# Optimization experiments

Measured on AMD Instinct MI355X. Metric: run time of the kernel, lower is better.

## Reference

```python
import jax, jax.numpy as jnp
import numpy as np

H = 16        # query heads
D = 4         # KV downsampling -> H//D = 4 kv heads
WINDOW = 1024 # sliding window
THETA = 10000.0


def _rope_cos_sin(L, dim):
    freqs = 1.0 / (THETA ** (jnp.arange(0, dim - 1, 2, dtype=jnp.float32) / dim))
    ang = jnp.arange(L, dtype=jnp.float32)[:, None] * freqs[None, :]  # (L, dim//2)
    return jnp.cos(ang), jnp.sin(ang)


def _apply_rope(x, cos, sin):
    # x: (N, h, L, dim); interleaved complex pairs (even=real, odd=imag)
    xr, xi = x[..., 0::2], x[..., 1::2]
    orr = xr * cos - xi * sin
    oii = xr * sin + xi * cos
    return jnp.stack([orr, oii], axis=-1).reshape(x.shape)


def setup_inputs() -> dict:
    key = jax.random.key(0)
    ks = jax.random.split(key, 5)
    N, L, E = 4, 2048, 2048
    return {
        "x": jax.random.normal(ks[0], (N, L, E), dtype=jnp.float32),
        "Wq": jax.random.normal(ks[1], (E, E), dtype=jnp.float32) * 0.02,
        "Wk": jax.random.normal(ks[2], (E // D, E), dtype=jnp.float32) * 0.02,
        "Wv": jax.random.normal(ks[3], (E // D, E), dtype=jnp.float32) * 0.02,
        "Wo": jax.random.normal(ks[4], (E, E), dtype=jnp.float32) * 0.02,
    }


def reference(x, Wq, Wk, Wv, Wo):
    N, L, E = x.shape
    dim = E // H  # 128 per-head dim (same for q and downsampled k/v)
    Hkv = H // D

    q = (x @ Wq.T).reshape(N, L, H, dim).transpose(0, 2, 1, 3)      # (N,H,L,d)
    k = (x @ Wk.T).reshape(N, L, Hkv, dim).transpose(0, 2, 1, 3)    # (N,Hkv,L,d)
    v = (x @ Wv.T).reshape(N, L, Hkv, dim).transpose(0, 2, 1, 3)

    cos, sin = _rope_cos_sin(L, dim)
    q = _apply_rope(q, cos, sin)
    k = _apply_rope(k, cos, sin)

    # GQA: expand kv heads (repeat_interleave along head axis)
    k = jnp.repeat(k, D, axis=1)  # (N,H,L,d)
    v = jnp.repeat(v, D, axis=1)

    scale = 1.0 / jnp.sqrt(jnp.float32(dim))
    attn = jnp.einsum("bhld,bhsd->bhls", q, k) * scale  # (N,H,L,L)

    i = jnp.arange(L)[:, None]
    j = jnp.arange(L)[None, :]
    allowed = (j <= i) & (j > i - WINDOW)  # causal + sliding window
    attn = jnp.where(allowed[None, None], attn, -jnp.inf)
    attn = jax.nn.softmax(attn, axis=-1)

    z = jnp.einsum("bhls,bhsd->bhld", attn, v)  # (N,H,L,d)
    z = z.transpose(0, 2, 1, 3).reshape(N, L, E)
    return z @ Wo.T
```

## Files before the change

### kernel.cpp

```cpp
#include <hip/hip_runtime.h>
#include <hip/hip_bf16.h>
#include <math.h>

typedef unsigned short u16;
typedef unsigned int u32;
typedef __attribute__((ext_vector_type(8))) short short8;
typedef __attribute__((ext_vector_type(8))) u16 ushort8;
typedef __attribute__((ext_vector_type(4))) float f32x4;
typedef __attribute__((ext_vector_type(16))) float f32x16;
typedef __attribute__((ext_vector_type(4))) u32 u32x4;

#define N_B 4
#define L_S 2048
#define E_D 2048
#define NH 16
#define HD 128
#define WIN 1024
#define QW 3072
#define LOG2E 1.4426950408889634f

static __device__ __forceinline__ u16 f32_bf16(float f) {
  u32 u = __builtin_bit_cast(u32, f);
  u = (u + 0x7fffu + ((u >> 16) & 1u)) >> 16;
  return (u16)u;
}
static __device__ __forceinline__ float bf16_f32(u16 h) {
  u32 u = ((u32)h) << 16;
  return __builtin_bit_cast(float, u);
}
static __device__ __forceinline__ u32 pack_bf16_pair(float lo, float hi) {
  __hip_bfloat162 h2 = __float22bfloat162_rn(make_float2(lo, hi));
  u32 r;
  __builtin_memcpy(&r, &h2, 4);
  return r;
}
static __device__ __forceinline__ void gload_lds16(const void* g, void* l) {
  __builtin_amdgcn_global_load_lds((__attribute__((address_space(1))) void*)g,
                                   (__attribute__((address_space(3))) void*)l, 16, 0, 0);
}

__global__ void k_cast(const float* __restrict__ src, u16* __restrict__ dst, int n8) {
  int i = blockIdx.x * blockDim.x + threadIdx.x;
  if (i >= n8) return;
  const float4* s = (const float4*)src + (size_t)i * 2;
  float4 a = s[0], b = s[1];
  ushort8 v;
  v[0] = f32_bf16(a.x); v[1] = f32_bf16(a.y); v[2] = f32_bf16(a.z); v[3] = f32_bf16(a.w);
  v[4] = f32_bf16(b.x); v[5] = f32_bf16(b.y); v[6] = f32_bf16(b.z); v[7] = f32_bf16(b.w);
  *((ushort8*)dst + i) = v;
}

__global__ void k_cast_w(const float* __restrict__ Wq, const float* __restrict__ Wk,
                         const float* __restrict__ Wv, const float* __restrict__ Wo,
                         u16* __restrict__ Wqkv, u16* __restrict__ Wob,
                         float* __restrict__ cs, float* __restrict__ sn) {
  int bb = blockIdx.x;
  if (bb >= 5120) {
    int idx = (bb - 5120) * 256 + threadIdx.x;
    int l = idx >> 6, f = idx & 63;
    float freq = exp2f(-(float)f * (13.287712379549449f / 64.0f));
    float ang = (float)l * freq;
    cs[idx] = cosf(ang);
    sn[idx] = sinf(ang);
    return;
  }
  const float* src;
  u16* dst;
  int base;
  if (bb < 2048)      { src = Wq; dst = Wqkv;                 base = bb; }
  else if (bb < 2560) { src = Wk; dst = Wqkv + 2048 * 2048;   base = bb - 2048; }
  else if (bb < 3072) { src = Wv; dst = Wqkv + 2560 * 2048;   base = bb - 2560; }
  else                { src = Wo; dst = Wob;                  base = bb - 3072; }
  int i = base * 256 + threadIdx.x;
  const float4* s = (const float4*)src + (size_t)i * 2;
  float4 a = s[0], b = s[1];
  ushort8 v;
  v[0] = f32_bf16(a.x); v[1] = f32_bf16(a.y); v[2] = f32_bf16(a.z); v[3] = f32_bf16(a.w);
  v[4] = f32_bf16(b.x); v[5] = f32_bf16(b.y); v[6] = f32_bf16(b.z); v[7] = f32_bf16(b.w);
  *((ushort8*)dst + i) = v;
}

__global__ void k_rope_k(u16* __restrict__ QKV, const float* __restrict__ cs,
                         const float* __restrict__ sn) {
  int idx = blockIdx.x * blockDim.x + threadIdx.x;
  int f = idx & 63;
  int rest = idx >> 6;
  int hh = rest & 3;
  int row = rest >> 2;
  int l = row & (L_S - 1);
  int col = E_D + hh * HD + 2 * f;
  u32* p = (u32*)(QKV + (size_t)row * QW + col);
  u32 v = *p;
  float xr = bf16_f32((u16)(v & 0xffffu));
  float xi = bf16_f32((u16)(v >> 16));
  float c = cs[l * 64 + f], s = sn[l * 64 + f];
  float orr = xr * c - xi * s;
  float oii = xr * s + xi * c;
  *p = (u32)f32_bf16(orr) | ((u32)f32_bf16(oii) << 16);
}

template <int OUT_F32, int BN>
__global__ __launch_bounds__(512, 1) void k_gemm8(
    const u16* __restrict__ A, int lda,
    const u16* __restrict__ B, int ldb,
    void* __restrict__ Cp, int ldc, int K) {
  constexpr int NF = BN / 64;
  constexpr int PB = BN / 128;
  constexpr int BBY = BN * 64;
  constexpr int LVM = 2 + PB;
  __shared__ __align__(16) u16 Ab[3 * 8192];
  __shared__ __align__(16) u16 Bb[3 * (BN * 32)];
  const int tid = threadIdx.x;
  const int lane = tid & 63, w = tid >> 6;
  const int lr = lane & 15, lg = lane >> 4;
  const int wm = w >> 2, wn = w & 3;
  const int fid = blockIdx.x;
  const int cc = fid & 7, l = fid >> 3;
  const int m0 = (cc * 4 + (l & 3)) * 256;
  const int n0 = (l >> 2) * BN;
  const int rswz = (lr & 6) << 3;

  const int r2 = tid >> 2;
  const int ce = (((tid & 3) * 16) ^ ((r2 & 6) << 3)) >> 1;
  auto STAGE_A = [&](int kt, int bb) {
#pragma unroll
    for (int rr = 0; rr < 2; ++rr)
      gload_lds16(A + (size_t)(m0 + rr * 128 + r2) * lda + kt * 32 + ce,
                  (char*)Ab + bb * 16384 + rr * 8192 + (w << 10));
  };
  auto STAGE_B = [&](int kt, int bb) {
#pragma unroll
    for (int rr = 0; rr < PB; ++rr)
      gload_lds16(B + (size_t)(n0 + rr * 128 + r2) * ldb + kt * 32 + ce,
                  (char*)Bb + bb * BBY + rr * 8192 + (w << 10));
  };

  f32x4 acc[8][NF];
  const f32x4 z4 = {0.f, 0.f, 0.f, 0.f};
#pragma unroll
  for (int mf = 0; mf < 8; ++mf)
#pragma unroll
    for (int nf = 0; nf < NF; ++nf) acc[mf][nf] = z4;

  const int nt = K >> 5;
  STAGE_A(0, 0); STAGE_B(0, 0);
  STAGE_A(1, 1); STAGE_B(1, 1);
  asm volatile("s_waitcnt vmcnt(%0)" :: "i"(LVM) : "memory");
  __builtin_amdgcn_sched_barrier(0);
  __builtin_amdgcn_s_barrier();
  __builtin_amdgcn_sched_barrier(0);

  int c3 = 0;
  for (int t = 0; t < nt; ++t) {
    int ib = c3 + 2; if (ib >= 3) ib -= 3;
    const char* Abt = (const char*)Ab + c3 * 16384;
    const char* Bbt = (const char*)Bb + c3 * BBY;
    short8 af[4], bf[NF];
#pragma unroll
    for (int nf = 0; nf < NF; ++nf) {
      int row = wn * (BN / 4) + nf * 16 + lr;
      bf[nf] = *(const short8*)(Bbt + row * 64 + ((lg * 16) ^ rswz));
    }
#pragma unroll
    for (int mf = 0; mf < 4; ++mf) {
      int row = wm * 128 + mf * 16 + lr;
      af[mf] = *(const short8*)(Abt + row * 64 + ((lg * 16) ^ rswz));
    }
    if (t + 2 < nt) STAGE_A(t + 2, ib);
    __builtin_amdgcn_sched_barrier(0);
    __builtin_amdgcn_s_barrier();
    asm volatile("s_waitcnt lgkmcnt(0)" ::: "memory");
    __builtin_amdgcn_sched_barrier(0);
    __builtin_amdgcn_s_setprio(1);
#pragma unroll
    for (int mf = 0; mf < 4; ++mf)
#pragma unroll
      for (int nf = 0; nf < NF; ++nf)
        acc[mf][nf] =
            __builtin_amdgcn_mfma_f32_16x16x32_bf16(af[mf], bf[nf], acc[mf][nf], 0, 0, 0);
    __builtin_amdgcn_s_setprio(0);
    __builtin_amdgcn_sched_barrier(0);
    __builtin_amdgcn_s_barrier();
    __builtin_amdgcn_sched_barrier(0);
#pragma unroll
    for (int mf = 0; mf < 4; ++mf) {
      int row = wm * 128 + 64 + mf * 16 + lr;
      af[mf] = *(const short8*)(Abt + row * 64 + ((lg * 16) ^ rswz));
    }
    if (t + 2 < nt) STAGE_B(t + 2, ib);
    if (t + 2 < nt)
      asm volatile("s_waitcnt vmcnt(%0)" :: "i"(LVM) : "memory");
    else
      asm volatile("s_waitcnt vmcnt(0)" ::: "memory");
    __builtin_amdgcn_sched_barrier(0);
    __builtin_amdgcn_s_barrier();
    asm volatile("s_waitcnt lgkmcnt(0)" ::: "memory");
    __builtin_amdgcn_sched_barrier(0);
    __builtin_amdgcn_s_setprio(1);
#pragma unroll
    for (int mf = 0; mf < 4; ++mf)
#pragma unroll
      for (int nf = 0; nf < NF; ++nf)
        acc[4 + mf][nf] =
            __builtin_amdgcn_mfma_f32_16x16x32_bf16(af[mf], bf[nf], acc[4 + mf][nf], 0, 0, 0);
    __builtin_amdgcn_s_setprio(0);
    __builtin_amdgcn_sched_barrier(0);
    __builtin_amdgcn_s_barrier();
    __builtin_amdgcn_sched_barrier(0);
    c3 = (c3 == 2) ? 0 : c3 + 1;
  }

#pragma unroll
  for (int mf = 0; mf < 8; ++mf)
#pragma unroll
    for (int nf = 0; nf < NF; ++nf)
#pragma unroll
      for (int j = 0; j < 4; ++j) {
        size_t r = (size_t)(m0 + wm * 128 + mf * 16 + lg * 4 + j);
        int c = n0 + wn * (BN / 4) + nf * 16 + lr;
        if (OUT_F32)
          ((float*)Cp)[r * ldc + c] = acc[mf][nf][j];
        else
          ((u16*)Cp)[r * ldc + c] = f32_bf16(acc[mf][nf][j]);
      }
}

__global__ __launch_bounds__(512, 2) void k_attn(u16* __restrict__ QKV,
                                                 const float* __restrict__ cs,
                                                 const float* __restrict__ sn) {
  const int bx = blockIdx.x, h = blockIdx.y, b = blockIdx.z;
  const int qb = (b >= 2) ? 7 - bx : bx;
  const int tid = threadIdx.x;
  const int lane = tid & 63, w = tid >> 6;
  const int l31 = lane & 31, hi = lane >> 5;
  const int kh = h >> 2;
  const int qs = qb * 256 + w * 32;
  __shared__ __align__(16) u16 Klds[2][64 * 128];
  __shared__ __align__(16) u16 Vt[2][128 * 64];
  const float SCL2 = 0.08838834764831845f * 1.4426950408889634f;
  const size_t bL = (size_t)b * L_S;
  const int q = qs + l31;
  const size_t rowQ = (bL + q) * QW + h * HD;
  short8 qf[8];
#pragma unroll
  for (int ds = 0; ds < 8; ++ds) {
    short8 qr = *(const short8*)(QKV + rowQ + ds * 16 + hi * 8);
    const int f0 = ds * 8 + hi * 4;
    float4 c4 = *(const float4*)(cs + (size_t)q * 64 + f0);
    float4 s4 = *(const float4*)(sn + (size_t)q * 64 + f0);
    ushort8 qo;
#pragma unroll
    for (int e = 0; e < 4; ++e) {
      float xr = bf16_f32((u16)qr[2 * e]);
      float xi = bf16_f32((u16)qr[2 * e + 1]);
      float co = (e == 0) ? c4.x : (e == 1) ? c4.y : (e == 2) ? c4.z : c4.w;
      float si = (e == 0) ? s4.x : (e == 1) ? s4.y : (e == 2) ? s4.z : s4.w;
      qo[2 * e]     = f32_bf16(xr * co - xi * si);
      qo[2 * e + 1] = f32_bf16(xr * si + xi * co);
    }
    qf[ds] = __builtin_bit_cast(short8, qo);
  }
  f32x16 o[4];
#pragma unroll
  for (int dt = 0; dt < 4; ++dt)
#pragma unroll
    for (int r = 0; r < 16; ++r) o[dt][r] = 0.f;
  float m2 = -3e38f, lsum = 0.f;
  int t0 = qb * 256 - (WIN - 1);
  if (t0 < 0) t0 = 0;
  t0 >>= 6;
  const int t1 = 4 * qb + 3;
  short8 vreg[2];

  auto ISSUE_K = [&](int t, int buf) {
    char* Kb = (char*)Klds + buf * 16384;
#pragma unroll
    for (int rr = 0; rr < 2; ++rr) {
      int row = rr * 32 + (tid >> 4);
      int colb = ((tid & 15) * 16) ^ ((row & 7) << 4);
      gload_lds16(QKV + (bL + t * 64 + row) * QW + E_D + kh * HD + (colb >> 1),
                  Kb + rr * 8192 + w * 1024 + (lane << 4));
    }
  };
  auto LOAD_V = [&](int t) {
#pragma unroll
    for (int rr = 0; rr < 2; ++rr)
      vreg[rr] = *(const short8*)(QKV + (bL + t * 64 + lane) * QW + E_D + 512 + kh * HD +
                                  ((w * 2 + rr) * 8));
  };
  auto WRITE_V = [&](int buf) {
    char* Vb = (char*)Vt + buf * 16384;
#pragma unroll
    for (int rr = 0; rr < 2; ++rr) {
      int db = (w * 2 + rr) * 8;
#pragma unroll
      for (int e = 0; e < 8; ++e)
        *(u16*)(Vb + ((((db + e) * 128) + lane * 2) ^ (e << 4))) = (u16)vreg[rr][e];
    }
  };

  LOAD_V(t0);
  ISSUE_K(t0, 0);
  __syncthreads();
  WRITE_V(0);
  int c = 0;

  for (int t = t0; t <= t1; ++t) {
    const int kv0 = t * 64;
    const bool lastt = (t == t1);
    if (!lastt) {
      ISSUE_K(t + 1, c ^ 1);
      LOAD_V(t + 1);
    }
    const bool act = (kv0 <= qs + 31) && (kv0 + 63 > qs - WIN);
    const bool full = (kv0 + 63 <= qs) && (kv0 > qs + 31 - WIN);
    u32x4 pa[4];
    if (act) {
      char* Kb = (char*)Klds + c * 16384;
      f32x16 s[2];
#pragma unroll
      for (int g = 0; g < 2; ++g)
#pragma unroll
        for (int r = 0; r < 16; ++r) s[g][r] = 0.f;
#pragma unroll
      for (int g = 0; g < 2; ++g) {
        const int r = g * 32 + l31;
        const int rsw = (r & 7) << 4;
#pragma unroll
        for (int ds = 0; ds < 8; ++ds) {
          short8 kf = *(const short8*)(Kb + (r * 256 + ((ds * 32 + hi * 16) ^ rsw)));
          s[g] = __builtin_amdgcn_mfma_f32_32x32x16_bf16(kf, qf[ds], s[g], 0, 0, 0);
        }
      }
      float v[2][16];
      float mx = -3e38f;
      if (full) {
#pragma unroll
        for (int g = 0; g < 2; ++g)
#pragma unroll
          for (int r = 0; r < 16; ++r) {
            float vv = s[g][r] * SCL2;
            v[g][r] = vv;
            mx = fmaxf(mx, vv);
          }
      } else {
#pragma unroll
        for (int g = 0; g < 2; ++g)
#pragma unroll
          for (int r = 0; r < 16; ++r) {
            int kg = kv0 + g * 32 + (r & 3) + 8 * (r >> 2) + 4 * hi;
            bool a = (kg <= q) && (kg > q - WIN);
            float vv = a ? s[g][r] * SCL2 : -3e38f;
            v[g][r] = vv;
            mx = fmaxf(mx, vv);
          }
      }
      mx = fmaxf(mx, __shfl_xor(mx, 32));
      if (__ballot(mx > m2 + 11.5415603f)) {
        float mn = fmaxf(m2, mx);
        float alpha = exp2f(m2 - mn);
        m2 = mn;
        lsum *= alpha;
#pragma unroll
        for (int r = 0; r < 16; ++r) {
          float alr = __shfl(alpha, (r & 3) + 8 * (r >> 2) + 4 * hi);
#pragma unroll
          for (int dt = 0; dt < 4; ++dt) o[dt][r] *= alr;
        }
      }
      float rs = 0.f;
      if (full) {
#pragma unroll
        for (int g = 0; g < 2; ++g)
#pragma unroll
          for (int r = 0; r < 16; ++r) {
            float pe = exp2f(v[g][r] - m2);
            v[g][r] = pe;
            rs += pe;
          }
      } else {
#pragma unroll
        for (int g = 0; g < 2; ++g)
#pragma unroll
          for (int r = 0; r < 16; ++r) {
            float pe = (v[g][r] > -1e37f) ? exp2f(v[g][r] - m2) : 0.f;
            v[g][r] = pe;
            rs += pe;
          }
      }
      rs += __shfl_xor(rs, 32);
      lsum += rs;
#pragma unroll
      for (int g = 0; g < 2; ++g) {
        u32 W[8];
#pragma unroll
        for (int qi = 0; qi < 4; ++qi) {
          W[2 * qi]     = pack_bf16_pair(v[g][4 * qi + 0], v[g][4 * qi + 1]);
          W[2 * qi + 1] = pack_bf16_pair(v[g][4 * qi + 2], v[g][4 * qi + 3]);
        }
        u32 R[4];
        R[0] = __shfl_xor(hi ? W[0] : W[2], 32);
        R[1] = __shfl_xor(hi ? W[1] : W[3], 32);
        R[2] = __shfl_xor(hi ? W[4] : W[6], 32);
        R[3] = __shfl_xor(hi ? W[5] : W[7], 32);
#pragma unroll
        for (int ksl = 0; ksl < 2; ++ksl) {
          u32x4 fr;
          if (hi == 0) {
            fr[0] = W[4 * ksl]; fr[1] = W[4 * ksl + 1];
            fr[2] = R[2 * ksl]; fr[3] = R[2 * ksl + 1];
          } else {
            fr[0] = R[2 * ksl]; fr[1] = R[2 * ksl + 1];
            fr[2] = W[4 * ksl + 2]; fr[3] = W[4 * ksl + 3];
          }
          pa[g * 2 + ksl] = fr;
        }
      }
    }
    __syncthreads();
    if (act) {
      char* Vb = (char*)Vt + c * 16384;
      __builtin_amdgcn_s_setprio(1);
#pragma unroll
      for (int dt = 0; dt < 4; ++dt) {
        const int d = dt * 32 + l31;
        const int dsw = (d & 7) << 4;
#pragma unroll
        for (int ks = 0; ks < 4; ++ks) {
          short8 vf = *(const short8*)(Vb + (d * 128 + ((ks * 32 + hi * 16) ^ dsw)));
          o[dt] = __builtin_amdgcn_mfma_f32_32x32x16_bf16(
              __builtin_bit_cast(short8, pa[ks]), vf, o[dt], 0, 0, 0);
        }
      }
      __builtin_amdgcn_s_setprio(0);
    }
    if (!lastt) WRITE_V(c ^ 1);
    c ^= 1;
  }
  float inv = 1.0f / lsum;
#pragma unroll
  for (int r = 0; r < 16; ++r) {
    int ridx = (r & 3) + 8 * (r >> 2) + 4 * hi;
    float invr = __shfl(inv, ridx);
    size_t rowO = (bL + qs + ridx) * QW + h * HD + l31;
#pragma unroll
    for (int dt = 0; dt < 4; ++dt)
      QKV[rowO + dt * 32] = f32_bf16(o[dt][r] * invr);
  }
}

extern "C" void kernel_launch(void* const* d_in, const int* in_sizes, int n_in,
                              void* d_out, int out_size, void* d_ws, size_t ws_size,
                              hipStream_t stream) {
  const float* x  = (const float*)d_in[0];
  const float* Wq = (const float*)d_in[1];
  const float* Wk = (const float*)d_in[2];
  const float* Wv = (const float*)d_in[3];
  const float* Wo = (const float*)d_in[4];
  char* ws = (char*)d_ws;
  if (ws_size < 105906176u) return;
  u16* xb    = (u16*)(ws);
  u16* Wqkv  = (u16*)(ws + 33554432);
  u16* Wob   = (u16*)(ws + 46137344);
  u16* QKV   = (u16*)(ws + 54525952);
  float* cs  = (float*)(ws + 104857600);
  float* sn  = (float*)(ws + 105381888);

  k_cast<<<8192, 256, 0, stream>>>(x, xb, 16777216 / 8);
  k_cast_w<<<5632, 256, 0, stream>>>(Wq, Wk, Wv, Wo, Wqkv, Wob, cs, sn);
  k_gemm8<0, 128><<<768, 512, 0, stream>>>(xb, 2048, Wqkv, 2048, QKV, QW, 2048);
  k_rope_k<<<8192, 256, 0, stream>>>(QKV, cs, sn);
  k_attn<<<dim3(8, 16, 4), 512, 0, stream>>>(QKV, cs, sn);
  k_gemm8<1, 256><<<256, 512, 0, stream>>>(QKV, QW, Wob, 2048, d_out, 2048, 2048);
}
```

Before: 351.4 us.

## Triple-buffer K tiles and single-buffer V with explicit vmcnt waits

Moves the attention kernel's K tile staging from double to triple buffering, so K is prefetched two tiles ahead via direct-to-LDS loads. V shrinks to a single LDS buffer, written after a second barrier. The full __syncthreads is replaced by manual s_waitcnt with partial vmcnt counts and raw s_barrier calls, so in-flight K loads need not drain at each iteration. This aims to hide global latency better, but it adds a barrier per iteration and depends on exact vmcnt accounting being correct.

```diff
diff --git a/kernel.cpp b/kernel.cpp
--- a/kernel.cpp
+++ b/kernel.cpp
@@ -235,8 +235,9 @@
   const int l31 = lane & 31, hi = lane >> 5;
   const int kh = h >> 2;
   const int qs = qb * 256 + w * 32;
-  __shared__ __align__(16) u16 Klds[2][64 * 128];
-  __shared__ __align__(16) u16 Vt[2][128 * 64];
+  __shared__ __align__(16) u16 Klds[3][64 * 128];
+  __shared__ __align__(16) u16 Vt[128 * 64];
+  char* Vb = (char*)Vt;
   const float SCL2 = 0.08838834764831845f * 1.4426950408889634f;
   const size_t bL = (size_t)b * L_S;
   const int q = qs + l31;
@@ -288,8 +289,7 @@
       vreg[rr] = *(const short8*)(QKV + (bL + t * 64 + lane) * QW + E_D + 512 + kh * HD +
                                   ((w * 2 + rr) * 8));
   };
-  auto WRITE_V = [&](int buf) {
-    char* Vb = (char*)Vt + buf * 16384;
+  auto WRITE_V = [&]() {
 #pragma unroll
     for (int rr = 0; rr < 2; ++rr) {
       int db = (w * 2 + rr) * 8;
@@ -300,23 +300,22 @@
   };
 
   LOAD_V(t0);
-  ISSUE_K(t0, 0);
+  ISSUE_K(t0, t0 % 3);
+  ISSUE_K(t0 + 1, (t0 + 1) % 3);
   __syncthreads();
-  WRITE_V(0);
-  int c = 0;
+  WRITE_V();
 
   for (int t = t0; t <= t1; ++t) {
     const int kv0 = t * 64;
-    const bool lastt = (t == t1);
-    if (!lastt) {
-      ISSUE_K(t + 1, c ^ 1);
-      LOAD_V(t + 1);
-    }
+    const bool haveV = (t + 1 <= t1);
+    const bool haveK = (t + 2 <= t1);
+    if (haveV) LOAD_V(t + 1);
+    if (haveK) ISSUE_K(t + 2, (t + 2) % 3);
     const bool act = (kv0 <= qs + 31) && (kv0 + 63 > qs - WIN);
     const bool full = (kv0 + 63 <= qs) && (kv0 > qs + 31 - WIN);
     u32x4 pa[4];
     if (act) {
-      char* Kb = (char*)Klds + c * 16384;
+      const char* Kb = (const char*)Klds + (t % 3) * 16384;
       f32x16 s[2];
 #pragma unroll
       for (int g = 0; g < 2; ++g)
@@ -417,9 +416,11 @@
         }
       }
     }
-    __syncthreads();
+    asm volatile("s_waitcnt lgkmcnt(0)" ::: "memory");
+    __builtin_amdgcn_sched_barrier(0);
+    __builtin_amdgcn_s_barrier();
+    __builtin_amdgcn_sched_barrier(0);
     if (act) {
-      char* Vb = (char*)Vt + c * 16384;
       __builtin_amdgcn_s_setprio(1);
 #pragma unroll
       for (int dt = 0; dt < 4; ++dt) {
@@ -434,8 +435,16 @@
       }
       __builtin_amdgcn_s_setprio(0);
     }
-    if (!lastt) WRITE_V(c ^ 1);
-    c ^= 1;
+    if (haveK)
+      asm volatile("s_waitcnt vmcnt(4)" ::: "memory");
+    else if (haveV)
+      asm volatile("s_waitcnt vmcnt(2)" ::: "memory");
+    else
+      asm volatile("s_waitcnt vmcnt(0)" ::: "memory");
+    __builtin_amdgcn_sched_barrier(0);
+    __builtin_amdgcn_s_barrier();
+    __builtin_amdgcn_sched_barrier(0);
+    if (haveV) WRITE_V();
   }
   float inv = 1.0f / lsum;
 #pragma unroll
```

Result: no change. 349.5 us (median of 3 runs) (-0.5%).
